# Kernel tuning notes

Measured on AMD Instinct MI355X. Metric: run time of the kernel, lower is better.

## Reference

```python
import jax, jax.numpy as jnp
import numpy as np

EPS = 1e-12

def _wn(v, g):
    # weight norm per output channel (axis 0): w[o] = g[o] * v[o] / ||v[o]||
    return g[:, None] * v / jnp.linalg.norm(v, axis=1, keepdims=True)

def _unit(x):
    # row-wise L2 normalize with clip, matching _normalize in source
    return x / jnp.clip(jnp.linalg.norm(x, axis=-1, keepdims=True), EPS)

def setup_inputs() -> dict:
    key = jax.random.key(0)
    ks = jax.random.split(key, 8)
    D, CD, K, T = 1024, 256, 8192, 16384
    return {
        "z": jax.random.normal(ks[0], (D, T), dtype=jnp.float32),
        "in_v": jax.random.normal(ks[1], (CD, D), dtype=jnp.float32) * 0.02,
        "in_g": jax.random.uniform(ks[2], (CD,), dtype=jnp.float32, minval=0.5, maxval=1.5),
        "in_b": jax.random.normal(ks[3], (CD,), dtype=jnp.float32) * 0.01,
        "out_v": jax.random.normal(ks[4], (D, CD), dtype=jnp.float32) * 0.02,
        "out_g": jax.random.uniform(ks[5], (D,), dtype=jnp.float32, minval=0.5, maxval=1.5),
        "out_b": jax.random.normal(ks[6], (D,), dtype=jnp.float32) * 0.01,
        "codebook": jax.random.normal(ks[7], (K, CD), dtype=jnp.float32),
    }

def reference(z, in_v, in_g, in_b, out_v, out_g, out_b, codebook):
    # in_proj: weight-normed 1x1 conv == matmul over channel dim
    z_e = _wn(in_v, in_g) @ z + in_b[:, None]            # (CD, T)
    # decode_latents
    enc = _unit(z_e.T)                                    # (T, CD)
    cb = _unit(codebook)                                  # (K, CD)
    # squared L2 distance via matmul-based cdist
    dist = (jnp.sum(enc * enc, axis=1, keepdims=True)
            - 2.0 * enc @ cb.T
            + jnp.sum(cb * cb, axis=1)[None, :])          # (T, K)
    indices = jnp.argmax(-dist, axis=1)                   # (T,)
    z_q = codebook[indices].T                             # (CD, T), raw codebook gather
    # straight-through estimator
    z_q = z_e + jax.lax.stop_gradient(z_q - z_e)
    # out_proj
    out = _wn(out_v, out_g) @ z_q + out_b[:, None]        # (D, T)
    return (out, indices)
```

## Files before the change

kernel.cpp:

```cpp
#include <hip/hip_runtime.h>
#include <hip/hip_bf16.h>
#include <math.h>

#define TDIM 16384
#define DDIM 1024
#define CDIM 256
#define KDIM 8192
#define KSPLIT 8

typedef unsigned short u16;
typedef __attribute__((ext_vector_type(8))) short bf16x8;
typedef __attribute__((ext_vector_type(8))) unsigned short us8;
typedef __attribute__((ext_vector_type(4))) float floatx4;

static const size_t OFF_WINH  = 0;
static const size_t OFF_WINL  = OFF_WINH  + (size_t)CDIM * DDIM / 2;
static const size_t OFF_WOUTH = OFF_WINL  + (size_t)CDIM * DDIM / 2;
static const size_t OFF_WOUTL = OFF_WOUTH + (size_t)DDIM * CDIM / 2;
static const size_t OFF_CBH   = OFF_WOUTL + (size_t)DDIM * CDIM / 2;
static const size_t OFF_CBL   = OFF_CBH   + (size_t)KDIM * CDIM / 2;
static const size_t OFF_C2    = OFF_CBL   + (size_t)KDIM * CDIM / 2;
static const size_t OFF_ZTH   = OFF_C2    + (size_t)KDIM;
static const size_t OFF_ZTL   = OFF_ZTH   + (size_t)TDIM * DDIM / 2;
static const size_t OFF_ZE    = OFF_ZTL   + (size_t)TDIM * DDIM / 2;
static const size_t OFF_PV    = OFF_ZE    + (size_t)CDIM * TDIM;
static const size_t OFF_PI    = OFF_PV    + (size_t)KSPLIT * TDIM;
static const size_t OFF_IDX   = OFF_PI    + (size_t)KSPLIT * TDIM;
static const size_t OFF_ETH   = OFF_ZTH;
static const size_t OFF_ETL   = OFF_ZTH + (size_t)TDIM * CDIM / 2;

static __device__ __forceinline__ u16 f2bf(float x) {
  __hip_bfloat16 h = __float2bfloat16(x);
  return *(u16*)&h;
}
static __device__ __forceinline__ float bf2f(u16 u) {
  __hip_bfloat16 h; *(u16*)&h = u;
  return __bfloat162float(h);
}

__global__ __launch_bounds__(256) void rownorm_split(
    const float* __restrict__ v, const float* __restrict__ g,
    u16* __restrict__ hi, u16* __restrict__ lo, float* __restrict__ c2,
    int ncols, int clip) {
  __shared__ float red[256];
  int row = blockIdx.x;
  const float* vr = v + (size_t)row * ncols;
  float s = 0.f;
  for (int j = threadIdx.x; j < ncols; j += 256) { float x = vr[j]; s += x * x; }
  red[threadIdx.x] = s;
  __syncthreads();
  for (int off = 128; off > 0; off >>= 1) {
    if (threadIdx.x < off) red[threadIdx.x] += red[threadIdx.x + off];
    __syncthreads();
  }
  float norm = sqrtf(red[0]);
  if (clip) norm = fmaxf(norm, 1e-12f);
  float scale = (g ? g[row] : 1.0f) / norm;
  float s2 = 0.f;
  for (int j = threadIdx.x; j < ncols; j += 256) {
    float y = vr[j] * scale;
    u16 hh = f2bf(y);
    u16 ll = f2bf(y - bf2f(hh));
    hi[(size_t)row * ncols + j] = hh;
    lo[(size_t)row * ncols + j] = ll;
    s2 += y * y;
  }
  if (c2) {
    __syncthreads();
    red[threadIdx.x] = s2;
    __syncthreads();
    for (int off = 128; off > 0; off >>= 1) {
      if (threadIdx.x < off) red[threadIdx.x] += red[threadIdx.x + off];
      __syncthreads();
    }
    if (threadIdx.x == 0) c2[row] = red[0];
  }
}

__global__ __launch_bounds__(256) void transpose_split_z(
    const float* __restrict__ z, u16* __restrict__ zth, u16* __restrict__ ztl) {
  __shared__ float tile[64][65];
  int t0 = blockIdx.x * 64, d0 = blockIdx.y * 64;
  int tl = threadIdx.x & 63, grp = threadIdx.x >> 6;
#pragma unroll
  for (int r = 0; r < 16; r++) {
    int d = grp * 16 + r;
    tile[d][tl] = z[(size_t)(d0 + d) * TDIM + t0 + tl];
  }
  __syncthreads();
#pragma unroll
  for (int r = 0; r < 16; r++) {
    int t = grp * 16 + r;
    float x = tile[tl][t];
    u16 h = f2bf(x);
    u16 l = f2bf(x - bf2f(h));
    zth[(size_t)(t0 + t) * DDIM + d0 + tl] = h;
    ztl[(size_t)(t0 + t) * DDIM + d0 + tl] = l;
  }
}

__global__ __launch_bounds__(256) void gemm_mfma_in(
    const u16* __restrict__ ah_g, const u16* __restrict__ al_g,
    const u16* __restrict__ bh_g, const u16* __restrict__ bl_g,
    const float* __restrict__ bias, float* __restrict__ C, int K) {
  __shared__ u16 Ah[128 * 32], Al[128 * 32];
  __shared__ u16 Bh[64 * 32],  Bl[64 * 32];
  int tid = threadIdx.x;
  int n0 = blockIdx.x * 64;
  int m0 = blockIdx.y * 128;
  int lane = tid & 63, wid = tid >> 6;
  int wr = wid >> 1, wc = wid & 1;
  int q = lane >> 4, mm = lane & 15;
  int h = tid & 1;
  int sr = ((tid >> 1) ^ (h << 2)) & 127;
  int ssw = (sr ^ (sr >> 2)) & 3;
  int o0 = sr * 32 + ((((h << 1))     ^ ssw) << 3);
  int o1 = sr * 32 + ((((h << 1) | 1) ^ ssw) << 3);
  int gcol = h * 16;
  int sb = ((tid >> 1) ^ (h << 2)) & 63;
  int ssb = (sb ^ (sb >> 2)) & 3;
  int p0 = sb * 32 + ((((h << 1))     ^ ssb) << 3);
  int p1 = sb * 32 + ((((h << 1) | 1) ^ ssb) << 3);
  int sm = (mm ^ (mm >> 2)) & 3;
  int cq = (q ^ sm) << 3;

  const floatx4 z4 = {0.f, 0.f, 0.f, 0.f};
  floatx4 acc[4][2];
#pragma unroll
  for (int i = 0; i < 4; i++)
#pragma unroll
    for (int j = 0; j < 2; j++) acc[i][j] = z4;

  for (int c0 = 0; c0 < K; c0 += 32) {
    const size_t ga = (size_t)(m0 + sr) * K + c0 + gcol;
    us8 a_h0 = *(const us8*)&ah_g[ga];
    us8 a_h1 = *(const us8*)&ah_g[ga + 8];
    us8 a_l0 = *(const us8*)&al_g[ga];
    us8 a_l1 = *(const us8*)&al_g[ga + 8];
    us8 b_h0, b_h1, b_l0, b_l1;
    if (tid < 128) {
      const size_t gb = (size_t)(n0 + sb) * K + c0 + gcol;
      b_h0 = *(const us8*)&bh_g[gb];
      b_h1 = *(const us8*)&bh_g[gb + 8];
      b_l0 = *(const us8*)&bl_g[gb];
      b_l1 = *(const us8*)&bl_g[gb + 8];
    }
    __syncthreads();
    *(us8*)&Ah[o0] = a_h0; *(us8*)&Ah[o1] = a_h1;
    *(us8*)&Al[o0] = a_l0; *(us8*)&Al[o1] = a_l1;
    if (tid < 128) {
      *(us8*)&Bh[p0] = b_h0; *(us8*)&Bh[p1] = b_h1;
      *(us8*)&Bl[p0] = b_l0; *(us8*)&Bl[p1] = b_l1;
    }
    __syncthreads();

    bf16x8 fa[4], fb[2];
#pragma unroll
    for (int i = 0; i < 4; i++)
      fa[i] = *(const bf16x8*)&Ah[(wr * 64 + i * 16 + mm) * 32 + cq];
#pragma unroll
    for (int j = 0; j < 2; j++)
      fb[j] = *(const bf16x8*)&Bh[(wc * 32 + j * 16 + mm) * 32 + cq];
#pragma unroll
    for (int i = 0; i < 4; i++)
#pragma unroll
      for (int j = 0; j < 2; j++)
        acc[i][j] = __builtin_amdgcn_mfma_f32_16x16x32_bf16(fa[i], fb[j], acc[i][j], 0, 0, 0);
#pragma unroll
    for (int i = 0; i < 4; i++) {
      bf16x8 fl = *(const bf16x8*)&Al[(wr * 64 + i * 16 + mm) * 32 + cq];
#pragma unroll
      for (int j = 0; j < 2; j++)
        acc[i][j] = __builtin_amdgcn_mfma_f32_16x16x32_bf16(fl, fb[j], acc[i][j], 0, 0, 0);
    }
#pragma unroll
    for (int j = 0; j < 2; j++) {
      bf16x8 fl = *(const bf16x8*)&Bl[(wc * 32 + j * 16 + mm) * 32 + cq];
#pragma unroll
      for (int i = 0; i < 4; i++)
        acc[i][j] = __builtin_amdgcn_mfma_f32_16x16x32_bf16(fa[i], fl, acc[i][j], 0, 0, 0);
    }
  }

#pragma unroll
  for (int i = 0; i < 4; i++) {
#pragma unroll
    for (int r = 0; r < 4; r++) {
      int m_loc = wr * 64 + i * 16 + q * 4 + r;
      float bb = bias[m0 + m_loc];
      float* crow = &C[(size_t)(m0 + m_loc) * TDIM + n0 + wc * 32 + mm];
#pragma unroll
      for (int j = 0; j < 2; j++) crow[j * 16] = acc[i][j][r] + bb;
    }
  }
}

__global__ __launch_bounds__(256) void gemm_mfma_bias(
    const u16* __restrict__ ah_g, const u16* __restrict__ al_g,
    const u16* __restrict__ bh_g, const u16* __restrict__ bl_g,
    const float* __restrict__ bias, float* __restrict__ C, int K) {
  __shared__ u16 Ah[128 * 32], Al[128 * 32];
  __shared__ u16 Bh[128 * 32], Bl[128 * 32];
  int tid = threadIdx.x;
  int n0 = blockIdx.x * 128;
  int m0 = blockIdx.y * 128;
  int lane = tid & 63, wid = tid >> 6;
  int wr = wid >> 1, wc = wid & 1;
  int q = lane >> 4, mm = lane & 15;
  int h = tid & 1;
  int sr = ((tid >> 1) ^ (h << 2)) & 127;
  int ssw = (sr ^ (sr >> 2)) & 3;
  int o0 = sr * 32 + ((((h << 1))     ^ ssw) << 3);
  int o1 = sr * 32 + ((((h << 1) | 1) ^ ssw) << 3);
  int gcol = h * 16;
  int sm = (mm ^ (mm >> 2)) & 3;
  int cq = (q ^ sm) << 3;

  const floatx4 z4 = {0.f, 0.f, 0.f, 0.f};
  floatx4 acc[4][4];
#pragma unroll
  for (int i = 0; i < 4; i++)
#pragma unroll
    for (int j = 0; j < 4; j++) acc[i][j] = z4;

  for (int c0 = 0; c0 < K; c0 += 32) {
    const size_t ga = (size_t)(m0 + sr) * K + c0 + gcol;
    const size_t gb = (size_t)(n0 + sr) * K + c0 + gcol;
    us8 a_h0 = *(const us8*)&ah_g[ga];
    us8 a_h1 = *(const us8*)&ah_g[ga + 8];
    us8 a_l0 = *(const us8*)&al_g[ga];
    us8 a_l1 = *(const us8*)&al_g[ga + 8];
    us8 b_h0 = *(const us8*)&bh_g[gb];
    us8 b_h1 = *(const us8*)&bh_g[gb + 8];
    us8 b_l0 = *(const us8*)&bl_g[gb];
    us8 b_l1 = *(const us8*)&bl_g[gb + 8];
    __syncthreads();
    *(us8*)&Ah[o0] = a_h0; *(us8*)&Ah[o1] = a_h1;
    *(us8*)&Al[o0] = a_l0; *(us8*)&Al[o1] = a_l1;
    *(us8*)&Bh[o0] = b_h0; *(us8*)&Bh[o1] = b_h1;
    *(us8*)&Bl[o0] = b_l0; *(us8*)&Bl[o1] = b_l1;
    __syncthreads();

    bf16x8 fa[4], fb[4];
#pragma unroll
    for (int i = 0; i < 4; i++)
      fa[i] = *(const bf16x8*)&Ah[(wr * 64 + i * 16 + mm) * 32 + cq];
#pragma unroll
    for (int j = 0; j < 4; j++)
      fb[j] = *(const bf16x8*)&Bh[(wc * 64 + j * 16 + mm) * 32 + cq];
#pragma unroll
    for (int i = 0; i < 4; i++)
#pragma unroll
      for (int j = 0; j < 4; j++)
        acc[i][j] = __builtin_amdgcn_mfma_f32_16x16x32_bf16(fa[i], fb[j], acc[i][j], 0, 0, 0);
#pragma unroll
    for (int i = 0; i < 4; i++) {
      bf16x8 fl = *(const bf16x8*)&Al[(wr * 64 + i * 16 + mm) * 32 + cq];
#pragma unroll
      for (int j = 0; j < 4; j++)
        acc[i][j] = __builtin_amdgcn_mfma_f32_16x16x32_bf16(fl, fb[j], acc[i][j], 0, 0, 0);
    }
#pragma unroll
    for (int j = 0; j < 4; j++) {
      bf16x8 fl = *(const bf16x8*)&Bl[(wc * 64 + j * 16 + mm) * 32 + cq];
#pragma unroll
      for (int i = 0; i < 4; i++)
        acc[i][j] = __builtin_amdgcn_mfma_f32_16x16x32_bf16(fa[i], fl, acc[i][j], 0, 0, 0);
    }
  }

#pragma unroll
  for (int i = 0; i < 4; i++) {
#pragma unroll
    for (int r = 0; r < 4; r++) {
      int m_loc = wr * 64 + i * 16 + q * 4 + r;
      float bb = bias[m0 + m_loc];
      float* crow = &C[(size_t)(m0 + m_loc) * TDIM + n0 + wc * 64 + mm];
#pragma unroll
      for (int j = 0; j < 4; j++) crow[j * 16] = acc[i][j][r] + bb;
    }
  }
}

__global__ __launch_bounds__(256) void finish_ze(
    const float* __restrict__ ze, u16* __restrict__ eth, u16* __restrict__ etl) {
  __shared__ float tile[256][33];
  __shared__ float red[8][32];
  __shared__ float invs[32];
  int t0 = blockIdx.x * 32;
  int tl = threadIdx.x & 31, grp = threadIdx.x >> 5;
  float s = 0.f;
  for (int c = grp * 32; c < grp * 32 + 32; c++) {
    float v = ze[(size_t)c * TDIM + t0 + tl];
    tile[c][tl] = v;
    s += v * v;
  }
  red[grp][tl] = s;
  __syncthreads();
  if (grp == 0) {
    float tot = 0.f;
#pragma unroll
    for (int gg = 0; gg < 8; gg++) tot += red[gg][tl];
    invs[tl] = 1.0f / fmaxf(sqrtf(tot), 1e-12f);
  }
  __syncthreads();
#pragma unroll
  for (int r = 0; r < 4; r++) {
    int t = grp * 4 + r;
    float iv = invs[t];
#pragma unroll
    for (int cc = 0; cc < 8; cc++) {
      int cd = cc * 32 + tl;
      float x = tile[cd][t] * iv;
      u16 hh = f2bf(x);
      u16 ll = f2bf(x - bf2f(hh));
      eth[(size_t)(t0 + t) * CDIM + cd] = hh;
      etl[(size_t)(t0 + t) * CDIM + cd] = ll;
    }
  }
}

__global__ __launch_bounds__(256) void dist_mfma(
    const u16* __restrict__ eth, const u16* __restrict__ etl,
    const u16* __restrict__ cbh, const u16* __restrict__ cbl,
    const float* __restrict__ c2, float* __restrict__ pv, int* __restrict__ pi) {
  __shared__ u16 Ah[128 * 32], Al[128 * 32];
  __shared__ u16 Bh[128 * 32], Bl[128 * 32];
  __shared__ float mv[2][128];
  __shared__ int   mi[2][128];
  int tid = threadIdx.x;
  int t0 = blockIdx.x * 128;
  int kbeg = blockIdx.y * (KDIM / KSPLIT);
  int lane = tid & 63, wid = tid >> 6;
  int wr = wid >> 1, wc = wid & 1;
  int q = lane >> 4, mm = lane & 15;
  int h = tid & 1;
  int sr = ((tid >> 1) ^ (h << 2)) & 127;
  int ssw = (sr ^ (sr >> 2)) & 3;
  int o0 = sr * 32 + ((((h << 1))     ^ ssw) << 3);
  int o1 = sr * 32 + ((((h << 1) | 1) ^ ssw) << 3);
  int gcol = h * 16;
  int sm = (mm ^ (mm >> 2)) & 3;
  int cq = (q ^ sm) << 3;

  float rbv[4]; int rbi[4];
#pragma unroll
  for (int i = 0; i < 4; i++) { rbv[i] = INFINITY; rbi[i] = 0x7fffffff; }

  const floatx4 z4 = {0.f, 0.f, 0.f, 0.f};
  for (int ktile = 0; ktile < KDIM / KSPLIT; ktile += 128) {
    int k0 = kbeg + ktile;
    floatx4 acc[4][4];
#pragma unroll
    for (int i = 0; i < 4; i++)
#pragma unroll
      for (int j = 0; j < 4; j++) acc[i][j] = z4;

    for (int c0 = 0; c0 < CDIM; c0 += 32) {
      const size_t ga = (size_t)(k0 + sr) * CDIM + c0 + gcol;
      const size_t gb = (size_t)(t0 + sr) * CDIM + c0 + gcol;
      us8 a_h0 = *(const us8*)&cbh[ga];
      us8 a_h1 = *(const us8*)&cbh[ga + 8];
      us8 a_l0 = *(const us8*)&cbl[ga];
      us8 a_l1 = *(const us8*)&cbl[ga + 8];
      us8 b_h0 = *(const us8*)&eth[gb];
      us8 b_h1 = *(const us8*)&eth[gb + 8];
      us8 b_l0 = *(const us8*)&etl[gb];
      us8 b_l1 = *(const us8*)&etl[gb + 8];
      __syncthreads();
      *(us8*)&Ah[o0] = a_h0; *(us8*)&Ah[o1] = a_h1;
      *(us8*)&Al[o0] = a_l0; *(us8*)&Al[o1] = a_l1;
      *(us8*)&Bh[o0] = b_h0; *(us8*)&Bh[o1] = b_h1;
      *(us8*)&Bl[o0] = b_l0; *(us8*)&Bl[o1] = b_l1;
      __syncthreads();

      bf16x8 fa[4], fb[4];
#pragma unroll
      for (int i = 0; i < 4; i++)
        fa[i] = *(const bf16x8*)&Ah[(wr * 64 + i * 16 + mm) * 32 + cq];
#pragma unroll
      for (int j = 0; j < 4; j++)
        fb[j] = *(const bf16x8*)&Bh[(wc * 64 + j * 16 + mm) * 32 + cq];
#pragma unroll
      for (int i = 0; i < 4; i++)
#pragma unroll
        for (int j = 0; j < 4; j++)
          acc[i][j] = __builtin_amdgcn_mfma_f32_16x16x32_bf16(fa[i], fb[j], acc[i][j], 0, 0, 0);
#pragma unroll
      for (int i = 0; i < 4; i++) {
        bf16x8 fl = *(const bf16x8*)&Al[(wr * 64 + i * 16 + mm) * 32 + cq];
#pragma unroll
        for (int j = 0; j < 4; j++)
          acc[i][j] = __builtin_amdgcn_mfma_f32_16x16x32_bf16(fl, fb[j], acc[i][j], 0, 0, 0);
      }
#pragma unroll
      for (int j = 0; j < 4; j++) {
        bf16x8 fl = *(const bf16x8*)&Bl[(wc * 64 + j * 16 + mm) * 32 + cq];
#pragma unroll
        for (int i = 0; i < 4; i++)
          acc[i][j] = __builtin_amdgcn_mfma_f32_16x16x32_bf16(fa[i], fl, acc[i][j], 0, 0, 0);
      }
    }

#pragma unroll
    for (int i = 0; i < 4; i++) {
#pragma unroll
      for (int r = 0; r < 4; r++) {
        int klocal = wr * 64 + i * 16 + q * 4 + r;
        float c2v = c2[k0 + klocal];
        int kg = k0 + klocal;
#pragma unroll
        for (int j = 0; j < 4; j++) {
          float s = c2v - 2.0f * acc[i][j][r];
          if (s < rbv[j]) { rbv[j] = s; rbi[j] = kg; }
        }
      }
    }
  }

#pragma unroll
  for (int j = 0; j < 4; j++) {
    float v = rbv[j]; int ii = rbi[j];
    float ov = __shfl_xor(v, 16, 64); int oi = __shfl_xor(ii, 16, 64);
    if (ov < v || (ov == v && oi < ii)) { v = ov; ii = oi; }
    ov = __shfl_xor(v, 32, 64); oi = __shfl_xor(ii, 32, 64);
    if (ov < v || (ov == v && oi < ii)) { v = ov; ii = oi; }
    rbv[j] = v; rbi[j] = ii;
  }
  if (q == 0) {
#pragma unroll
    for (int j = 0; j < 4; j++) {
      mv[wr][wc * 64 + j * 16 + mm] = rbv[j];
      mi[wr][wc * 64 + j * 16 + mm] = rbi[j];
    }
  }
  __syncthreads();
  if (tid < 128) {
    float v0 = mv[0][tid]; int i0 = mi[0][tid];
    float v1 = mv[1][tid]; int i1 = mi[1][tid];
    if (v1 < v0 || (v1 == v0 && i1 < i0)) { v0 = v1; i0 = i1; }
    pv[(size_t)blockIdx.y * TDIM + t0 + tid] = v0;
    pi[(size_t)blockIdx.y * TDIM + t0 + tid] = i0;
  }
}

__global__ __launch_bounds__(256) void merge_argmin(
    const float* __restrict__ pv, const int* __restrict__ pi,
    int* __restrict__ idx, float* __restrict__ idxf) {
  int t = blockIdx.x * 256 + threadIdx.x;
  float bv = INFINITY; int bi = 0x7fffffff;
  for (int s = 0; s < KSPLIT; s++) {
    float v = pv[(size_t)s * TDIM + t];
    int ii = pi[(size_t)s * TDIM + t];
    if (v < bv || (v == bv && ii < bi)) { bv = v; bi = ii; }
  }
  idx[t] = bi;
  idxf[t] = (float)bi;
}

__global__ __launch_bounds__(256) void gather_split(
    const int* __restrict__ idx, const float* __restrict__ cb,
    u16* __restrict__ zqh, u16* __restrict__ zql) {
  int t = blockIdx.x * 4 + (threadIdx.x >> 6);
  int c4 = (threadIdx.x & 63) * 4;
  int k = idx[t];
  float4 x = *(const float4*)&cb[(size_t)k * CDIM + c4];
  u16 h0 = f2bf(x.x), h1 = f2bf(x.y), h2 = f2bf(x.z), h3 = f2bf(x.w);
  u16 l0 = f2bf(x.x - bf2f(h0)), l1 = f2bf(x.y - bf2f(h1));
  u16 l2 = f2bf(x.z - bf2f(h2)), l3 = f2bf(x.w - bf2f(h3));
  ushort4 hv = {h0, h1, h2, h3}, lv = {l0, l1, l2, l3};
  *(ushort4*)&zqh[(size_t)t * CDIM + c4] = hv;
  *(ushort4*)&zql[(size_t)t * CDIM + c4] = lv;
}

extern "C" void kernel_launch(void* const* d_in, const int* in_sizes, int n_in,
                              void* d_out, int out_size, void* d_ws, size_t ws_size,
                              hipStream_t stream) {
  const float* z     = (const float*)d_in[0];
  const float* in_v  = (const float*)d_in[1];
  const float* in_g  = (const float*)d_in[2];
  const float* in_b  = (const float*)d_in[3];
  const float* out_v = (const float*)d_in[4];
  const float* out_g = (const float*)d_in[5];
  const float* out_b = (const float*)d_in[6];
  const float* cb    = (const float*)d_in[7];

  float* ws    = (float*)d_ws;
  u16*   winh  = (u16*)(ws + OFF_WINH);
  u16*   winl  = (u16*)(ws + OFF_WINL);
  u16*   wouth = (u16*)(ws + OFF_WOUTH);
  u16*   woutl = (u16*)(ws + OFF_WOUTL);
  u16*   cbh   = (u16*)(ws + OFF_CBH);
  u16*   cbl   = (u16*)(ws + OFF_CBL);
  float* c2    = ws + OFF_C2;
  u16*   zth   = (u16*)(ws + OFF_ZTH);
  u16*   ztl   = (u16*)(ws + OFF_ZTL);
  float* z_e   = ws + OFF_ZE;
  float* pv    = ws + OFF_PV;
  int*   pi    = (int*)(ws + OFF_PI);
  int*   idxw  = (int*)(ws + OFF_IDX);
  u16*   eth   = (u16*)(ws + OFF_ETH);
  u16*   etl   = (u16*)(ws + OFF_ETL);
  u16*   zqh   = eth;
  u16*   zql   = etl;

  float* outp = (float*)d_out;
  float* idxf = outp + (size_t)DDIM * TDIM;

  rownorm_split<<<CDIM, 256, 0, stream>>>(in_v, in_g, winh, winl, nullptr, DDIM, 0);
  rownorm_split<<<DDIM, 256, 0, stream>>>(out_v, out_g, wouth, woutl, nullptr, CDIM, 0);
  rownorm_split<<<KDIM, 256, 0, stream>>>(cb, nullptr, cbh, cbl, c2, CDIM, 1);

  transpose_split_z<<<dim3(TDIM / 64, DDIM / 64), 256, 0, stream>>>(z, zth, ztl);

  gemm_mfma_in<<<dim3(TDIM / 64, CDIM / 128), 256, 0, stream>>>(
      winh, winl, zth, ztl, in_b, z_e, DDIM);

  finish_ze<<<TDIM / 32, 256, 0, stream>>>(z_e, eth, etl);

  dist_mfma<<<dim3(TDIM / 128, KSPLIT), 256, 0, stream>>>(eth, etl, cbh, cbl, c2, pv, pi);
  merge_argmin<<<TDIM / 256, 256, 0, stream>>>(pv, pi, idxw, idxf);

  gather_split<<<TDIM / 4, 256, 0, stream>>>(idxw, cb, zqh, zql);

  gemm_mfma_bias<<<dim3(TDIM / 128, DDIM / 128), 256, 0, stream>>>(
      wouth, woutl, zqh, zql, out_b, outp, CDIM);
}
```

Measured before the change: 461.0 us.

## Restructure codebook distance kernel with resident encoder tile and double-buffered codebook loads

The distance kernel now runs 512 threads per block over 256-row codebook tiles. The encoder high-part tile (128x256) stays resident in shared memory for the whole block, and the codebook hi/lo and encoder lo slices are double-buffered, with global loads for the next step issued before the current MFMA work. This removes one of the two barriers per k-step and the repeated reloads of the encoder tile, trading them for much more LDS per block, which may limit occupancy. The final min-reduction now merges four wave rows instead of two.

```diff
diff --git a/kernel.cpp b/kernel.cpp
--- a/kernel.cpp
+++ b/kernel.cpp
@@ -320,101 +320,138 @@
   }
 }
 
-__global__ __launch_bounds__(256) void dist_mfma(
+__global__ __launch_bounds__(512, 2) void dist_mfma(
     const u16* __restrict__ eth, const u16* __restrict__ etl,
     const u16* __restrict__ cbh, const u16* __restrict__ cbl,
     const float* __restrict__ c2, float* __restrict__ pv, int* __restrict__ pi) {
-  __shared__ u16 Ah[128 * 32], Al[128 * 32];
-  __shared__ u16 Bh[128 * 32], Bl[128 * 32];
-  __shared__ float mv[2][128];
-  __shared__ int   mi[2][128];
+  __shared__ u16 Bh[128 * 256];
+  __shared__ u16 Ah[2][256 * 32];
+  __shared__ u16 Al[2][256 * 32];
+  __shared__ u16 Bls[2][128 * 32];
+  __shared__ float mv[4][128];
+  __shared__ int   mi[4][128];
+
   int tid = threadIdx.x;
   int t0 = blockIdx.x * 128;
   int kbeg = blockIdx.y * (KDIM / KSPLIT);
   int lane = tid & 63, wid = tid >> 6;
-  int wr = wid >> 1, wc = wid & 1;
+  int wk = wid >> 1, wt = wid & 1;
   int q = lane >> 4, mm = lane & 15;
-  int h = tid & 1;
-  int sr = ((tid >> 1) ^ (h << 2)) & 127;
-  int ssw = (sr ^ (sr >> 2)) & 3;
-  int o0 = sr * 32 + ((((h << 1))     ^ ssw) << 3);
-  int o1 = sr * 32 + ((((h << 1) | 1) ^ ssw) << 3);
-  int gcol = h * 16;
-  int sm = (mm ^ (mm >> 2)) & 3;
-  int cq = (q ^ sm) << 3;
+  int sm2 = (mm ^ (mm >> 2)) & 3;
+  int cq2 = (q ^ sm2) << 3;
+  int sm5 = sm2 | (((mm >> 1) & 1) << 2);
+
+  int rA = tid >> 2;
+  int gA = tid & 3;
+  int sswA = (rA ^ (rA >> 2)) & 3;
+  int colA = (gA ^ sswA) << 3;
+  int ldsA = rA * 32 + (gA << 3);
+
+  for (int it = 0; it < 8; ++it) {
+    int gi = it * 512 + tid;
+    int r = gi >> 5, p5 = gi & 31;
+    int f5 = ((r ^ (r >> 2)) & 3) | (((r >> 1) & 1) << 2);
+    us8 v = *(const us8*)&eth[(size_t)(t0 + r) * CDIM + ((p5 ^ f5) << 3)];
+    *(us8*)&Bh[r * 256 + (p5 << 3)] = v;
+  }
+
+  {
+    const size_t ga = (size_t)(kbeg + rA) * CDIM + colA;
+    us8 ah0 = *(const us8*)&cbh[ga];
+    us8 ah1 = *(const us8*)&cbh[ga + (size_t)128 * CDIM];
+    us8 al0 = *(const us8*)&cbl[ga];
+    us8 al1 = *(const us8*)&cbl[ga + (size_t)128 * CDIM];
+    us8 bl0 = *(const us8*)&etl[(size_t)(t0 + rA) * CDIM + colA];
+    *(us8*)&Ah[0][ldsA] = ah0; *(us8*)&Ah[0][ldsA + 4096] = ah1;
+    *(us8*)&Al[0][ldsA] = al0; *(us8*)&Al[0][ldsA + 4096] = al1;
+    *(us8*)&Bls[0][ldsA] = bl0;
+  }
+  __syncthreads();
 
   float rbv[4]; int rbi[4];
 #pragma unroll
-  for (int i = 0; i < 4; i++) { rbv[i] = INFINITY; rbi[i] = 0x7fffffff; }
+  for (int j = 0; j < 4; j++) { rbv[j] = INFINITY; rbi[j] = 0x7fffffff; }
 
   const floatx4 z4 = {0.f, 0.f, 0.f, 0.f};
-  for (int ktile = 0; ktile < KDIM / KSPLIT; ktile += 128) {
-    int k0 = kbeg + ktile;
-    floatx4 acc[4][4];
+  floatx4 acc[4][4];
+#pragma unroll
+  for (int i = 0; i < 4; i++)
+#pragma unroll
+    for (int j = 0; j < 4; j++) acc[i][j] = z4;
+
+  int cur = 0;
+  for (int n = 0; n < 32; ++n) {
+    int cc = n & 7;
+
+    us8 ah0, ah1, al0, al1, bl0;
+    if (n < 31) {
+      int n1 = n + 1;
+      int k0n = kbeg + (n1 >> 3) * 256;
+      int c0n = (n1 & 7) * 32;
+      const size_t ga = (size_t)(k0n + rA) * CDIM + c0n + colA;
+      ah0 = *(const us8*)&cbh[ga];
+      ah1 = *(const us8*)&cbh[ga + (size_t)128 * CDIM];
+      al0 = *(const us8*)&cbl[ga];
+      al1 = *(const us8*)&cbl[ga + (size_t)128 * CDIM];
+      bl0 = *(const us8*)&etl[(size_t)(t0 + rA) * CDIM + c0n + colA];
+    }
+
+    bf16x8 fah[4], fbh[4];
 #pragma unroll
     for (int i = 0; i < 4; i++)
-#pragma unroll
-      for (int j = 0; j < 4; j++) acc[i][j] = z4;
-
-    for (int c0 = 0; c0 < CDIM; c0 += 32) {
-      const size_t ga = (size_t)(k0 + sr) * CDIM + c0 + gcol;
-      const size_t gb = (size_t)(t0 + sr) * CDIM + c0 + gcol;
-      us8 a_h0 = *(const us8*)&cbh[ga];
-      us8 a_h1 = *(const us8*)&cbh[ga + 8];
-      us8 a_l0 = *(const us8*)&cbl[ga];
-      us8 a_l1 = *(const us8*)&cbl[ga + 8];
-      us8 b_h0 = *(const us8*)&eth[gb];
-      us8 b_h1 = *(const us8*)&eth[gb + 8];
-      us8 b_l0 = *(const us8*)&etl[gb];
-      us8 b_l1 = *(const us8*)&etl[gb + 8];
-      __syncthreads();
-      *(us8*)&Ah[o0] = a_h0; *(us8*)&Ah[o1] = a_h1;
-      *(us8*)&Al[o0] = a_l0; *(us8*)&Al[o1] = a_l1;
-      *(us8*)&Bh[o0] = b_h0; *(us8*)&Bh[o1] = b_h1;
-      *(us8*)&Bl[o0] = b_l0; *(us8*)&Bl[o1] = b_l1;
-      __syncthreads();
-
-      bf16x8 fa[4], fb[4];
+      fah[i] = *(const bf16x8*)&Ah[cur][(wk * 64 + i * 16 + mm) * 32 + cq2];
+#pragma unroll
+    for (int j = 0; j < 4; j++)
+      fbh[j] = *(const bf16x8*)&Bh[(wt * 64 + j * 16 + mm) * 256 +
+                                   ((((cc << 2) | q) ^ sm5) << 3)];
+#pragma unroll
+    for (int i = 0; i < 4; i++)
+#pragma unroll
+      for (int j = 0; j < 4; j++)
+        acc[i][j] = __builtin_amdgcn_mfma_f32_16x16x32_bf16(fah[i], fbh[j], acc[i][j], 0, 0, 0);
+#pragma unroll
+    for (int i = 0; i < 4; i++) {
+      bf16x8 fl = *(const bf16x8*)&Al[cur][(wk * 64 + i * 16 + mm) * 32 + cq2];
+#pragma unroll
+      for (int j = 0; j < 4; j++)
+        acc[i][j] = __builtin_amdgcn_mfma_f32_16x16x32_bf16(fl, fbh[j], acc[i][j], 0, 0, 0);
+    }
+#pragma unroll
+    for (int j = 0; j < 4; j++) {
+      bf16x8 fl = *(const bf16x8*)&Bls[cur][(wt * 64 + j * 16 + mm) * 32 + cq2];
 #pragma unroll
       for (int i = 0; i < 4; i++)
-        fa[i] = *(const bf16x8*)&Ah[(wr * 64 + i * 16 + mm) * 32 + cq];
-#pragma unroll
-      for (int j = 0; j < 4; j++)
-        fb[j] = *(const bf16x8*)&Bh[(wc * 64 + j * 16 + mm) * 32 + cq];
-#pragma unroll
-      for (int i = 0; i < 4; i++)
-#pragma unroll
-        for (int j = 0; j < 4; j++)
-          acc[i][j] = __builtin_amdgcn_mfma_f32_16x16x32_bf16(fa[i], fb[j], acc[i][j], 0, 0, 0);
+        acc[i][j] = __builtin_amdgcn_mfma_f32_16x16x32_bf16(fah[i], fl, acc[i][j], 0, 0, 0);
+    }
+
+    if (n < 31) {
+      int nb = cur ^ 1;
+      *(us8*)&Ah[nb][ldsA] = ah0; *(us8*)&Ah[nb][ldsA + 4096] = ah1;
+      *(us8*)&Al[nb][ldsA] = al0; *(us8*)&Al[nb][ldsA + 4096] = al1;
+      *(us8*)&Bls[nb][ldsA] = bl0;
+    }
+    __syncthreads();
+    cur ^= 1;
+
+    if (cc == 7) {
+      int k0 = kbeg + (n >> 3) * 256;
 #pragma unroll
       for (int i = 0; i < 4; i++) {
-        bf16x8 fl = *(const bf16x8*)&Al[(wr * 64 + i * 16 + mm) * 32 + cq];
-#pragma unroll
-        for (int j = 0; j < 4; j++)
-          acc[i][j] = __builtin_amdgcn_mfma_f32_16x16x32_bf16(fl, fb[j], acc[i][j], 0, 0, 0);
-      }
-#pragma unroll
-      for (int j = 0; j < 4; j++) {
-        bf16x8 fl = *(const bf16x8*)&Bl[(wc * 64 + j * 16 + mm) * 32 + cq];
-#pragma unroll
-        for (int i = 0; i < 4; i++)
-          acc[i][j] = __builtin_amdgcn_mfma_f32_16x16x32_bf16(fa[i], fl, acc[i][j], 0, 0, 0);
-      }
-    }
-
-#pragma unroll
-    for (int i = 0; i < 4; i++) {
-#pragma unroll
-      for (int r = 0; r < 4; r++) {
-        int klocal = wr * 64 + i * 16 + q * 4 + r;
-        float c2v = c2[k0 + klocal];
-        int kg = k0 + klocal;
-#pragma unroll
-        for (int j = 0; j < 4; j++) {
-          float s = c2v - 2.0f * acc[i][j][r];
-          if (s < rbv[j]) { rbv[j] = s; rbi[j] = kg; }
+#pragma unroll
+        for (int r4 = 0; r4 < 4; r4++) {
+          int kg = k0 + wk * 64 + i * 16 + q * 4 + r4;
+          float c2v = c2[kg];
+#pragma unroll
+          for (int j = 0; j < 4; j++) {
+            float s = c2v - 2.0f * acc[i][j][r4];
+            if (s < rbv[j]) { rbv[j] = s; rbi[j] = kg; }
+          }
         }
       }
+#pragma unroll
+      for (int i = 0; i < 4; i++)
+#pragma unroll
+        for (int j = 0; j < 4; j++) acc[i][j] = z4;
     }
   }
 
@@ -430,15 +467,18 @@
   if (q == 0) {
 #pragma unroll
     for (int j = 0; j < 4; j++) {
-      mv[wr][wc * 64 + j * 16 + mm] = rbv[j];
-      mi[wr][wc * 64 + j * 16 + mm] = rbi[j];
+      mv[wk][wt * 64 + j * 16 + mm] = rbv[j];
+      mi[wk][wt * 64 + j * 16 + mm] = rbi[j];
     }
   }
   __syncthreads();
   if (tid < 128) {
     float v0 = mv[0][tid]; int i0 = mi[0][tid];
-    float v1 = mv[1][tid]; int i1 = mi[1][tid];
-    if (v1 < v0 || (v1 == v0 && i1 < i0)) { v0 = v1; i0 = i1; }
+#pragma unroll
+    for (int w = 1; w < 4; w++) {
+      float v1 = mv[w][tid]; int i1 = mi[w][tid];
+      if (v1 < v0 || (v1 == v0 && i1 < i0)) { v0 = v1; i0 = i1; }
+    }
     pv[(size_t)blockIdx.y * TDIM + t0 + tid] = v0;
     pi[(size_t)blockIdx.y * TDIM + t0 + tid] = i0;
   }
@@ -518,7 +558,7 @@
 
   finish_ze<<<TDIM / 32, 256, 0, stream>>>(z_e, eth, etl);
 
-  dist_mfma<<<dim3(TDIM / 128, KSPLIT), 256, 0, stream>>>(eth, etl, cbh, cbl, c2, pv, pi);
+  dist_mfma<<<dim3(TDIM / 128, KSPLIT), 512, 0, stream>>>(eth, etl, cbh, cbl, c2, pv, pi);
   merge_argmin<<<TDIM / 256, 256, 0, stream>>>(pv, pi, idxw, idxf);
 
   gather_split<<<TDIM / 4, 256, 0, stream>>>(idxw, cb, zqh, zql);
```

New measurement: 435.1 us. 5.6% less time.
